# Performance work log

Hardware: AMD Instinct MI355X
Metric: run time of the kernel (lower is better)

Reference implementation:

```python
import jax, jax.numpy as jnp
import numpy as np
import math

B, T, V, A, D = 8, 128, 32000, 64, 256
NS, S, H = 16, 128, 4
HD = D // H
SCALE = math.sqrt(HD)


def _ln(x, g, b):
    m = x.mean(-1, keepdims=True)
    xc = x - m
    v = (xc * xc).mean(-1, keepdims=True)
    return xc * jax.lax.rsqrt(v + 1e-5) * g + b


def setup_inputs() -> dict:
    key = jax.random.key(0)
    ks = iter(jax.random.split(key, 64))
    def w(shape, s=0.02):
        return jax.random.normal(next(ks), shape, jnp.float32) * s
    return dict(
        idx=jax.random.randint(next(ks), (B, T), 0, V),
        emb=w((V, D)), pos=w((S, D)),
        Wsens=w((D, NS * D)), bsens=jnp.zeros((NS * D,), jnp.float32),
        Wfb=w((V, D)), bfb=jnp.zeros((D,), jnp.float32),
        Wfg=w((2 * D, D)), bfg=jnp.zeros((D,), jnp.float32),
        bind=w((NS, D)),
        anet=w((2, A, A)),
        Wg=w((2, 2 * D, D)), bg=jnp.zeros((2, D), jnp.float32),
        Wc=w((2, D, D)), bc=jnp.zeros((2, D), jnp.float32),
        lng=jnp.ones((2, D), jnp.float32), lnb=jnp.zeros((2, D), jnp.float32),
        cmix=jnp.ones((2,), jnp.float32) / 2, aimp=w((A,)),
        Wq=w((D, D)), bq=jnp.zeros((D,), jnp.float32),
        Wk=w((D, D)), bk=jnp.zeros((D,), jnp.float32),
        Wv=w((D, D)), bv=jnp.zeros((D,), jnp.float32),
        Wo=w((D, D)), bo=jnp.zeros((D,), jnp.float32),
        Wmg=w((2 * D, D)), bmg=jnp.zeros((D,), jnp.float32),
        mlng=jnp.ones((D,), jnp.float32), mlnb=jnp.zeros((D,), jnp.float32),
        Wa1=w((D, 2 * D)), ba1=jnp.zeros((2 * D,), jnp.float32),
        Wa2=w((2 * D, V)), ba2=jnp.zeros((V,), jnp.float32),
    )


def _forward(idx, emb, pos, Wsens, bsens, Wfb, bfb, Wfg, bfg, bind, anet,
             Wg, bg, Wc, bc, lng, lnb, cmix, aimp, Wq, bq, Wk, bk, Wv, bv,
             Wo, bo, Wmg, bmg, mlng, mlnb, Wa1, ba1, Wa2, ba2):
    percepts = emb[idx] + pos[:T][None]            # [B,T,D]
    iw = jax.nn.softmax(aimp)                      # [A]
    cw = jax.nn.softmax(cmix)                      # [2]
    sig_bind = jax.nn.sigmoid(bind)                # [NS,D]
    slot_ids = jnp.arange(S)

    def step(carry, pt):
        agents, prev_logits, mem, t = carry
        # feedback gating of percept
        fb = prev_logits @ Wfb + bfb
        fg = jax.nn.sigmoid(jnp.concatenate([fb, pt], -1) @ Wfg + bfg)
        mod = pt * (1 + fg)
        sens = (mod @ Wsens + bsens).reshape(B, NS, D) * sig_bind
        agents = agents.at[:, :NS].add(sens)
        # two swarm channels, mixed
        new = 0.
        for c in range(2):
            inter = jnp.einsum('ij,bjd->bid', anet[c], agents)
            cand = jax.nn.gelu(inter @ Wc[c] + bc[c], approximate=False)
            gate = jax.nn.sigmoid(jnp.concatenate([agents, inter], -1) @ Wg[c] + bg[c])
            new = new + cw[c] * _ln(gate * cand + (1 - gate) * agents, lng[c], lnb[c])
        agents = new
        cons = jnp.einsum('bad,a->bd', agents, iw)  # [B,D]
        # holographic memory attention over valid slots (< t)
        Q = (cons @ Wq + bq).reshape(B, 1, H, HD)
        K = (mem @ Wk + bk).reshape(B, S, H, HD)
        Vv = (mem @ Wv + bv).reshape(B, S, H, HD)
        scores = jnp.einsum('bqhd,bshd->bhqs', Q, K) / SCALE  # [B,H,1,S]
        valid = slot_ids < t
        scores = jnp.where(valid[None, None, None, :], scores, -1e9)
        attn = jax.nn.softmax(scores, -1)
        rec = jnp.einsum('bhqs,bshd->bqhd', attn, Vv).reshape(B, D)
        rec = rec @ Wo + bo
        mgate = jax.nn.sigmoid(jnp.concatenate([cons, rec], -1) @ Wmg + bmg)
        attended = _ln(cons + mgate * rec, mlng, mlnb)
        cons = jnp.where(t > 0, attended, cons)
        # write detached consensus to slot t (T == MEMORY_SLOTS)
        mem = jax.lax.dynamic_update_slice(
            mem, jax.lax.stop_gradient(cons)[:, None, :], (0, t, 0))
        h = jax.nn.gelu(cons @ Wa1 + ba1, approximate=False)
        logits = h @ Wa2 + ba2
        return (agents, jax.lax.stop_gradient(logits), mem, t + 1), logits

    carry0 = (jnp.zeros((B, A, D), jnp.float32),
              jnp.zeros((B, V), jnp.float32),
              jnp.zeros((B, S, D), jnp.float32),
              jnp.int32(0))
    _, logits = jax.lax.scan(step, carry0, percepts.transpose(1, 0, 2))
    return logits.transpose(1, 0, 2)  # [B,T,V]


def reference(idx, emb, pos, Wsens, bsens, Wfb, bfb, Wfg, bfg, bind, anet,
              Wg, bg, Wc, bc, lng, lnb, cmix, aimp, Wq, bq, Wk, bk, Wv, bv,
              Wo, bo, Wmg, bmg, mlng, mlnb, Wa1, ba1, Wa2, ba2):
    return _forward(idx, emb, pos, Wsens, bsens, Wfb, bfb, Wfg, bfg, bind,
                    anet, Wg, bg, Wc, bc, lng, lnb, cmix, aimp, Wq, bq, Wk,
                    bk, Wv, bv, Wo, bo, Wmg, bmg, mlng, mlnb, Wa1, ba1,
                    Wa2, ba2)
```

## Files before the change

kernel.cpp:

```cpp
#include <hip/hip_runtime.h>
#include <math.h>

#define DEV __device__ __forceinline__

constexpr int B = 8, T = 128, V = 32000, A = 64, D = 256, NS = 16, S = 128, H = 4, HD = 64;
constexpr int D2 = 2 * D;

DEV float sigm(float x) { return 1.0f / (1.0f + expf(-x)); }
DEV float geluf(float x) { return 0.5f * x * (1.0f + erff(x * 0.7071067811865476f)); }

DEV float blk_sum256(float v, float* red) {
  #pragma unroll
  for (int o = 32; o > 0; o >>= 1) v += __shfl_down(v, o, 64);
  int lane = threadIdx.x & 63, wid = threadIdx.x >> 6;
  __syncthreads();
  if (lane == 0) red[wid] = v;
  __syncthreads();
  return red[0] + red[1] + red[2] + red[3];
}


__global__ __launch_bounds__(256) void k_setup(const float* __restrict__ aimp,
                                               const float* __restrict__ cmix,
                                               const float* __restrict__ bind,
                                               float* __restrict__ iw, float* __restrict__ cwv,
                                               float* __restrict__ sigbind) {
  int tid = threadIdx.x;
  if (tid < 64) {
    float v = aimp[tid];
    float m = v;
    #pragma unroll
    for (int o = 32; o > 0; o >>= 1) m = fmaxf(m, __shfl_xor(m, o, 64));
    float e = expf(v - m);
    float s = e;
    #pragma unroll
    for (int o = 32; o > 0; o >>= 1) s += __shfl_xor(s, o, 64);
    iw[tid] = e / s;
  }
  if (tid == 0) {
    float a = cmix[0], b = cmix[1], m = fmaxf(a, b);
    float ea = expf(a - m), eb = expf(b - m);
    cwv[0] = ea / (ea + eb);
    cwv[1] = eb / (ea + eb);
  }
  for (int i = tid; i < NS * D; i += 256) sigbind[i] = sigm(bind[i]);
}

__global__ __launch_bounds__(256) void k_percepts(const int* __restrict__ idx,
                                                  const float* __restrict__ emb,
                                                  const float* __restrict__ pos,
                                                  float* __restrict__ P) {
  int i = blockIdx.x * 256 + threadIdx.x;
  if (i < B * T * D) {
    int d = i & (D - 1);
    int bt = i / D;
    int t = bt & (T - 1);
    P[i] = emb[(size_t)idx[bt] * D + d] + pos[t * D + d];
  }
}

__global__ __launch_bounds__(256) void k_cvec(const float* __restrict__ Wfb,
                                              const float* __restrict__ ba2,
                                              const float* __restrict__ bfb,
                                              float* __restrict__ cvec) {
  int j = blockIdx.x, tid = threadIdx.x;
  float s = 0.f;
  for (int v = tid; v < V; v += 256) s += ba2[v] * Wfb[(size_t)v * D + j];
  __shared__ float red[256];
  red[tid] = s;
  __syncthreads();
  for (int o = 128; o > 0; o >>= 1) {
    if (tid < o) red[tid] += red[tid + o];
    __syncthreads();
  }
  if (tid == 0) cvec[j] = red[0] + bfb[j];
}

__global__ __launch_bounds__(256) void k_mpart(const float* __restrict__ Wa2,
                                               const float* __restrict__ Wfb,
                                               float* __restrict__ part) {
  int it = blockIdx.y;
  int vc = blockIdx.x;
  int j = threadIdx.x;
  int i0 = it * 32, v0 = vc * 2000;
  __shared__ float a_l[32 * 125];
  float acc[32];
  #pragma unroll
  for (int r = 0; r < 32; r++) acc[r] = 0.f;
  for (int vb = 0; vb < 2000; vb += 125) {
    for (int l = threadIdx.x; l < 32 * 125; l += 256) {
      int r = l / 125, c = l - r * 125;
      a_l[l] = Wa2[(size_t)(i0 + r) * V + v0 + vb + c];
    }
    __syncthreads();
    for (int c = 0; c < 125; c++) {
      float w = Wfb[(size_t)(v0 + vb + c) * D + j];
      #pragma unroll
      for (int r = 0; r < 32; r++) acc[r] += a_l[r * 125 + c] * w;
    }
    __syncthreads();
  }
  for (int r = 0; r < 32; r++) part[((size_t)vc * D2 + i0 + r) * D + j] = acc[r];
}

__global__ __launch_bounds__(256) void k_mreduce(const float* __restrict__ part,
                                                 float* __restrict__ M) {
  int i = blockIdx.x, j = threadIdx.x;
  float s = 0.f;
  for (int vc = 0; vc < 16; vc++) s += part[((size_t)vc * D2 + i) * D + j];
  M[i * D + j] = s;
}

__global__ __launch_bounds__(256) void k_step0(const float* __restrict__ P,
                                               const float* __restrict__ bfb,
                                               const float* __restrict__ Wfg,
                                               const float* __restrict__ bfg,
                                               float* __restrict__ agents,
                                               float* __restrict__ mod) {
  int b = blockIdx.x, tid = threadIdx.x;
  for (int i = b * (A * D) + tid; i < (b + 1) * (A * D); i += 256) agents[i] = 0.f;
  __shared__ float cat[512];
  cat[tid] = bfb[tid];
  cat[256 + tid] = P[(b * T + 0) * D + tid];
  __syncthreads();
  float acc = bfg[tid];
  for (int k = 0; k < 512; k++) acc += cat[k] * Wfg[k * D + tid];
  float fg = sigm(acc);
  float pt = cat[256 + tid];
  mod[b * D + tid] = pt * (1.f + fg);
}


__global__ __launch_bounds__(256) void k_stepB(const float* __restrict__ Wsens,
                                               const float* __restrict__ bsens,
                                               const float* __restrict__ sigbind,
                                               const float* __restrict__ anet,
                                               const float* __restrict__ mod,
                                               float* __restrict__ agents,
                                               float* __restrict__ inter) {
  int b = blockIdx.y;
  int dc = blockIdx.x;
  int d0 = dc * 32;
  int tid = threadIdx.x;
  __shared__ float mod_l[256];
  __shared__ float ag_l[64][33];
  __shared__ float an_l[2 * 64 * 64];
  mod_l[tid] = mod[b * D + tid];
  for (int l = tid; l < 2 * 64 * 64; l += 256) an_l[l] = anet[l];
  for (int l = tid; l < 64 * 32; l += 256) {
    int j = l >> 5, dl = l & 31;
    ag_l[j][dl] = agents[(b * A + j) * D + d0 + dl];
  }
  __syncthreads();
  for (int l = tid; l < NS * 32; l += 256) {
    int j = l >> 5, dl = l & 31;
    int col = j * D + d0 + dl;
    float acc = bsens[col];
    for (int k = 0; k < D; k++) acc += mod_l[k] * Wsens[k * (NS * D) + col];
    float nv = ag_l[j][dl] + acc * sigbind[col];
    ag_l[j][dl] = nv;
    agents[(b * A + j) * D + d0 + dl] = nv;
  }
  __syncthreads();
  for (int l = tid; l < 2 * 64 * 32; l += 256) {
    int c = l >> 11;
    int rem = l & 2047;
    int i = rem >> 5, dl = rem & 31;
    const float* an = &an_l[(c * 64 + i) * 64];
    float acc = 0.f;
    #pragma unroll 8
    for (int j = 0; j < 64; j++) acc += an[j] * ag_l[j][dl];
    inter[(((c * B) + b) * A + i) * D + d0 + dl] = acc;
  }
}

__global__ __launch_bounds__(256) void k_stepC(const float* __restrict__ Wc,
                                               const float* __restrict__ bc,
                                               const float* __restrict__ Wg,
                                               const float* __restrict__ bg,
                                               const float* __restrict__ lng,
                                               const float* __restrict__ lnb,
                                               const float* __restrict__ cwv,
                                               const float* __restrict__ inter,
                                               float* __restrict__ agents) {
  int r0 = blockIdx.x * 4;
  int tid = threadIdx.x;
  __shared__ float ag_l[4][256];
  __shared__ float in_l[4][2][256];
  __shared__ float red[4];
  for (int rr = 0; rr < 4; rr++) {
    ag_l[rr][tid] = agents[(r0 + rr) * D + tid];
    in_l[rr][0][tid] = inter[(r0 + rr) * D + tid];
    in_l[rr][1][tid] = inter[B * A * D + (r0 + rr) * D + tid];
  }
  __syncthreads();
  float c0[4] = {0, 0, 0, 0}, c1[4] = {0, 0, 0, 0};
  float g0[4] = {0, 0, 0, 0}, g1[4] = {0, 0, 0, 0};
  for (int k = 0; k < 256; k++) {
    float wc0 = Wc[k * D + tid];
    float wc1 = Wc[D * D + k * D + tid];
    float wg0 = Wg[k * D + tid];
    float wg1 = Wg[D2 * D + k * D + tid];
    #pragma unroll
    for (int rr = 0; rr < 4; rr++) {
      c0[rr] += in_l[rr][0][k] * wc0;
      c1[rr] += in_l[rr][1][k] * wc1;
      g0[rr] += ag_l[rr][k] * wg0;
      g1[rr] += ag_l[rr][k] * wg1;
    }
  }
  for (int k = 0; k < 256; k++) {
    float wg0 = Wg[(256 + k) * D + tid];
    float wg1 = Wg[D2 * D + (256 + k) * D + tid];
    #pragma unroll
    for (int rr = 0; rr < 4; rr++) {
      g0[rr] += in_l[rr][0][k] * wg0;
      g1[rr] += in_l[rr][1][k] * wg1;
    }
  }
  float cw0 = cwv[0], cw1 = cwv[1];
  float bc0 = bc[tid], bc1 = bc[D + tid];
  float bg0 = bg[tid], bg1 = bg[D + tid];
  float lg0 = lng[tid], lg1 = lng[D + tid];
  float lb0 = lnb[tid], lb1 = lnb[D + tid];
  for (int rr = 0; rr < 4; rr++) {
    float cand0 = geluf(c0[rr] + bc0);
    float cand1 = geluf(c1[rr] + bc1);
    float gate0 = sigm(g0[rr] + bg0);
    float gate1 = sigm(g1[rr] + bg1);
    float a = ag_l[rr][tid];
    float v0 = gate0 * cand0 + (1.f - gate0) * a;
    float v1 = gate1 * cand1 + (1.f - gate1) * a;
    float s0 = blk_sum256(v0, red);
    float q0 = blk_sum256(v0 * v0, red);
    float s1 = blk_sum256(v1, red);
    float q1 = blk_sum256(v1 * v1, red);
    float m0 = s0 * (1.f / 256.f), var0 = q0 * (1.f / 256.f) - m0 * m0;
    float m1 = s1 * (1.f / 256.f), var1 = q1 * (1.f / 256.f) - m1 * m1;
    float ln0 = (v0 - m0) * rsqrtf(var0 + 1e-5f) * lg0 + lb0;
    float ln1 = (v1 - m1) * rsqrtf(var1 + 1e-5f) * lg1 + lb1;
    agents[(r0 + rr) * D + tid] = cw0 * ln0 + cw1 * ln1;
  }
}

__global__ __launch_bounds__(256) void k_stepD(
    int t, const float* __restrict__ P, const float* __restrict__ iw,
    const float* __restrict__ Wq, const float* __restrict__ bq,
    const float* __restrict__ Wk, const float* __restrict__ bk,
    const float* __restrict__ Wv, const float* __restrict__ bv,
    const float* __restrict__ Wo, const float* __restrict__ bo,
    const float* __restrict__ Wmg, const float* __restrict__ bmg,
    const float* __restrict__ mlng, const float* __restrict__ mlnb,
    const float* __restrict__ Wa1, const float* __restrict__ ba1,
    const float* __restrict__ M, const float* __restrict__ cvec,
    const float* __restrict__ Wfg, const float* __restrict__ bfg,
    const float* __restrict__ agents, float* __restrict__ Kc, float* __restrict__ Vc,
    float* __restrict__ Hall, float* __restrict__ mod) {
  int b = blockIdx.x, tid = threadIdx.x;
  __shared__ float cons_l[256], q_l[256], o_l[256], cf_l[256], h_l[512];
  __shared__ float sc_l[4][128];
  __shared__ float den_l[4];
  __shared__ float red[4];
  float acc = 0.f;
  for (int a = 0; a < A; a++) acc += iw[a] * agents[(b * A + a) * D + tid];
  cons_l[tid] = acc;
  __syncthreads();
  float consd = acc;
  float cfd;
  if (t > 0) {
    float q = bq[tid];
    for (int k = 0; k < 256; k++) q += cons_l[k] * Wq[k * D + tid];
    q_l[tid] = q;
    __syncthreads();
    for (int p = tid; p < 4 * 128; p += 256) {
      int h = p >> 7, s = p & 127;
      if (s < t) {
        const float* krow = &Kc[(b * S + s) * D + h * HD];
        const float* qh = &q_l[h * HD];
        float sc = 0.f;
        #pragma unroll 8
        for (int e = 0; e < HD; e++) sc += qh[e] * krow[e];
        sc_l[h][s] = sc * 0.125f;
      }
    }
    __syncthreads();
    int h = tid >> 6, lane = tid & 63;
    {
      float m = -1e30f;
      for (int s = lane; s < t; s += 64) m = fmaxf(m, sc_l[h][s]);
      #pragma unroll
      for (int o = 32; o > 0; o >>= 1) m = fmaxf(m, __shfl_xor(m, o, 64));
      float sum = 0.f;
      for (int s = lane; s < t; s += 64) {
        float e = expf(sc_l[h][s] - m);
        sc_l[h][s] = e;
        sum += e;
      }
      #pragma unroll
      for (int o = 32; o > 0; o >>= 1) sum += __shfl_xor(sum, o, 64);
      if (lane == 0) den_l[h] = sum;
    }
    __syncthreads();
    float r = 0.f;
    for (int s = 0; s < t; s++) r += sc_l[h][s] * Vc[(b * S + s) * D + tid];
    r /= den_l[h];
    __syncthreads();
    q_l[tid] = r;
    __syncthreads();
    float o = bo[tid];
    for (int k = 0; k < 256; k++) o += q_l[k] * Wo[k * D + tid];
    o_l[tid] = o;
    __syncthreads();
    float mg = bmg[tid];
    for (int k = 0; k < 256; k++) mg += cons_l[k] * Wmg[k * D + tid];
    for (int k = 0; k < 256; k++) mg += o_l[k] * Wmg[(256 + k) * D + tid];
    mg = sigm(mg);
    float val = consd + mg * o;
    float s1 = blk_sum256(val, red);
    float s2 = blk_sum256(val * val, red);
    float mean = s1 * (1.f / 256.f), var = s2 * (1.f / 256.f) - mean * mean;
    cfd = (val - mean) * rsqrtf(var + 1e-5f) * mlng[tid] + mlnb[tid];
  } else {
    cfd = consd;
  }
  __syncthreads();
  cf_l[tid] = cfd;
  __syncthreads();
  float kk = bk[tid], vv = bv[tid];
  for (int k = 0; k < 256; k++) {
    float c = cf_l[k];
    kk += c * Wk[k * D + tid];
    vv += c * Wv[k * D + tid];
  }
  Kc[(b * S + t) * D + tid] = kk;
  Vc[(b * S + t) * D + tid] = vv;
  for (int m = tid; m < 512; m += 256) {
    float hh = ba1[m];
    for (int k = 0; k < 256; k++) hh += cf_l[k] * Wa1[k * D2 + m];
    hh = geluf(hh);
    h_l[m] = hh;
    Hall[((size_t)b * T + t) * D2 + m] = hh;
  }
  __syncthreads();
  if (t < T - 1) {
    float fb = cvec[tid];
    for (int k = 0; k < 512; k++) fb += h_l[k] * M[k * D + tid];
    float ptn = P[(b * T + t + 1) * D + tid];
    q_l[tid] = fb;
    o_l[tid] = ptn;
    __syncthreads();
    float fg = bfg[tid];
    for (int k = 0; k < 256; k++) fg += q_l[k] * Wfg[k * D + tid];
    for (int k = 0; k < 256; k++) fg += o_l[k] * Wfg[(256 + k) * D + tid];
    fg = sigm(fg);
    mod[b * D + tid] = ptn * (1.f + fg);
  }
}

__global__ __launch_bounds__(256) void k_logits(const float* __restrict__ Hall,
                                                const float* __restrict__ Wa2,
                                                const float* __restrict__ ba2,
                                                float* __restrict__ out) {
  int rt = blockIdx.y;
  int v = blockIdx.x * 256 + threadIdx.x;
  const float* hrow = Hall + (size_t)rt * 32 * D2;
  float acc[32];
  float bb = ba2[v];
  #pragma unroll
  for (int r = 0; r < 32; r++) acc[r] = bb;
  for (int k = 0; k < D2; k++) {
    float w = Wa2[(size_t)k * V + v];
    #pragma unroll
    for (int r = 0; r < 32; r++) acc[r] += hrow[r * D2 + k] * w;
  }
  for (int r = 0; r < 32; r++) out[(size_t)(rt * 32 + r) * V + v] = acc[r];
}


extern "C" void kernel_launch(void* const* d_in, const int* in_sizes, int n_in,
                              void* d_out, int out_size, void* d_ws, size_t ws_size,
                              hipStream_t stream) {
  const int* idx = (const int*)d_in[0];
  const float* emb = (const float*)d_in[1];
  const float* pos = (const float*)d_in[2];
  const float* Wsens = (const float*)d_in[3];
  const float* bsens = (const float*)d_in[4];
  const float* Wfb = (const float*)d_in[5];
  const float* bfb = (const float*)d_in[6];
  const float* Wfg = (const float*)d_in[7];
  const float* bfg = (const float*)d_in[8];
  const float* bind = (const float*)d_in[9];
  const float* anet = (const float*)d_in[10];
  const float* Wg = (const float*)d_in[11];
  const float* bg = (const float*)d_in[12];
  const float* Wc = (const float*)d_in[13];
  const float* bc = (const float*)d_in[14];
  const float* lng = (const float*)d_in[15];
  const float* lnb = (const float*)d_in[16];
  const float* cmix = (const float*)d_in[17];
  const float* aimp = (const float*)d_in[18];
  const float* Wq = (const float*)d_in[19];
  const float* bq = (const float*)d_in[20];
  const float* Wk = (const float*)d_in[21];
  const float* bk = (const float*)d_in[22];
  const float* Wv = (const float*)d_in[23];
  const float* bv = (const float*)d_in[24];
  const float* Wo = (const float*)d_in[25];
  const float* bo = (const float*)d_in[26];
  const float* Wmg = (const float*)d_in[27];
  const float* bmg = (const float*)d_in[28];
  const float* mlng = (const float*)d_in[29];
  const float* mlnb = (const float*)d_in[30];
  const float* Wa1 = (const float*)d_in[31];
  const float* ba1 = (const float*)d_in[32];
  const float* Wa2 = (const float*)d_in[33];
  const float* ba2 = (const float*)d_in[34];

  float* ws = (float*)d_ws;
  float* M = ws;
  float* cvec = ws + 131072;
  float* iw = ws + 131328;
  float* cw = ws + 131392;
  float* sigbind = ws + 131456;
  float* P = ws + 135552;
  float* agents = ws + 397696;
  float* inter = ws + 528768;
  float* mod = ws + 790912;
  float* Kc = ws + 792960;
  float* Vc = ws + 1055104;
  float* Hall = ws + 1317248;
  float* Mpart = ws + 1841536;

  k_setup<<<1, 256, 0, stream>>>(aimp, cmix, bind, iw, cw, sigbind);
  k_percepts<<<dim3((B * T * D + 255) / 256), 256, 0, stream>>>(idx, emb, pos, P);
  k_cvec<<<256, 256, 0, stream>>>(Wfb, ba2, bfb, cvec);
  k_mpart<<<dim3(16, 16), 256, 0, stream>>>(Wa2, Wfb, Mpart);
  k_mreduce<<<512, 256, 0, stream>>>(Mpart, M);
  k_step0<<<B, 256, 0, stream>>>(P, bfb, Wfg, bfg, agents, mod);

  for (int t = 0; t < T; t++) {
    k_stepB<<<dim3(8, B), 256, 0, stream>>>(Wsens, bsens, sigbind, anet, mod, agents, inter);
    k_stepC<<<128, 256, 0, stream>>>(Wc, bc, Wg, bg, lng, lnb, cw, inter, agents);
    k_stepD<<<B, 256, 0, stream>>>(t, P, iw, Wq, bq, Wk, bk, Wv, bv, Wo, bo, Wmg, bmg,
                                   mlng, mlnb, Wa1, ba1, M, cvec, Wfg, bfg, agents, Kc, Vc,
                                   Hall, mod);
  }
  k_logits<<<dim3(125, 32), 256, 0, stream>>>(Hall, Wa2, ba2, (float*)d_out);
}
```

Before: 26.39 ms.

## Replace per-step kernel launches with a cooperative persistent kernel and prefolded weights

Swaps the 3×128 per-timestep kernel launches for a single cooperative persistent kernel of 256 blocks that uses grid.sync between phases. The work inside each step is spread over many more blocks. Weight products are folded ahead of time (M·Wfg, Wo·Wmg, P·Wfg, bias vectors) to shorten the serial chain, and K is stored transposed. The goal is to remove launch overhead and the poor parallelism of 8-block stages, at the cost of many grid-wide barriers per step and some reassociated floating-point arithmetic.

```diff
diff --git a/kernel.cpp b/kernel.cpp
--- a/kernel.cpp
+++ b/kernel.cpp
@@ -1,5 +1,8 @@
 #include <hip/hip_runtime.h>
+#include <hip/hip_cooperative_groups.h>
 #include <math.h>
+
+namespace cg = cooperative_groups;
 
 #define DEV __device__ __forceinline__
 
@@ -8,16 +11,6 @@
 
 DEV float sigm(float x) { return 1.0f / (1.0f + expf(-x)); }
 DEV float geluf(float x) { return 0.5f * x * (1.0f + erff(x * 0.7071067811865476f)); }
-
-DEV float blk_sum256(float v, float* red) {
-  #pragma unroll
-  for (int o = 32; o > 0; o >>= 1) v += __shfl_down(v, o, 64);
-  int lane = threadIdx.x & 63, wid = threadIdx.x >> 6;
-  __syncthreads();
-  if (lane == 0) red[wid] = v;
-  __syncthreads();
-  return red[0] + red[1] + red[2] + red[3];
-}
 
 
 __global__ __launch_bounds__(256) void k_setup(const float* __restrict__ aimp,
@@ -82,12 +75,12 @@
   int it = blockIdx.y;
   int vc = blockIdx.x;
   int j = threadIdx.x;
-  int i0 = it * 32, v0 = vc * 2000;
+  int i0 = it * 32, v0 = vc * 4000;
   __shared__ float a_l[32 * 125];
   float acc[32];
   #pragma unroll
   for (int r = 0; r < 32; r++) acc[r] = 0.f;
-  for (int vb = 0; vb < 2000; vb += 125) {
+  for (int vb = 0; vb < 4000; vb += 125) {
     for (int l = threadIdx.x; l < 32 * 125; l += 256) {
       int r = l / 125, c = l - r * 125;
       a_l[l] = Wa2[(size_t)(i0 + r) * V + v0 + vb + c];
@@ -107,253 +100,399 @@
                                                  float* __restrict__ M) {
   int i = blockIdx.x, j = threadIdx.x;
   float s = 0.f;
-  for (int vc = 0; vc < 16; vc++) s += part[((size_t)vc * D2 + i) * D + j];
+  for (int vc = 0; vc < 8; vc++) s += part[((size_t)vc * D2 + i) * D + j];
   M[i * D + j] = s;
 }
 
-__global__ __launch_bounds__(256) void k_step0(const float* __restrict__ P,
-                                               const float* __restrict__ bfb,
-                                               const float* __restrict__ Wfg,
-                                               const float* __restrict__ bfg,
-                                               float* __restrict__ agents,
-                                               float* __restrict__ mod) {
-  int b = blockIdx.x, tid = threadIdx.x;
-  for (int i = b * (A * D) + tid; i < (b + 1) * (A * D); i += 256) agents[i] = 0.f;
-  __shared__ float cat[512];
-  cat[tid] = bfb[tid];
-  cat[256 + tid] = P[(b * T + 0) * D + tid];
+__global__ __launch_bounds__(256) void k_gemmK256(const float* __restrict__ Am,
+                                                  const float* __restrict__ Bm,
+                                                  float* __restrict__ C, int I) {
+  int r0 = blockIdx.x * 8;
+  int tid = threadIdx.x;
+  __shared__ float a_l[8][256];
+  for (int i = tid; i < 8 * 256; i += 256) a_l[i >> 8][i & 255] = Am[(r0 + (i >> 8)) * 256 + (i & 255)];
   __syncthreads();
-  float acc = bfg[tid];
-  for (int k = 0; k < 512; k++) acc += cat[k] * Wfg[k * D + tid];
-  float fg = sigm(acc);
-  float pt = cat[256 + tid];
-  mod[b * D + tid] = pt * (1.f + fg);
-}
-
-
-__global__ __launch_bounds__(256) void k_stepB(const float* __restrict__ Wsens,
-                                               const float* __restrict__ bsens,
-                                               const float* __restrict__ sigbind,
-                                               const float* __restrict__ anet,
-                                               const float* __restrict__ mod,
-                                               float* __restrict__ agents,
-                                               float* __restrict__ inter) {
-  int b = blockIdx.y;
-  int dc = blockIdx.x;
-  int d0 = dc * 32;
+  float acc[8] = {0, 0, 0, 0, 0, 0, 0, 0};
+  for (int k = 0; k < 256; k++) {
+    float bv = Bm[k * 256 + tid];
+    #pragma unroll
+    for (int r = 0; r < 8; r++) acc[r] += a_l[r][k] * bv;
+  }
+  for (int r = 0; r < 8; r++) C[(r0 + r) * 256 + tid] = acc[r];
+}
+
+__global__ __launch_bounds__(256) void k_vecmat(const float* __restrict__ a,
+                                                const float* __restrict__ Bm,
+                                                const float* __restrict__ bias,
+                                                float* __restrict__ out) {
   int tid = threadIdx.x;
-  __shared__ float mod_l[256];
-  __shared__ float ag_l[64][33];
-  __shared__ float an_l[2 * 64 * 64];
-  mod_l[tid] = mod[b * D + tid];
-  for (int l = tid; l < 2 * 64 * 64; l += 256) an_l[l] = anet[l];
-  for (int l = tid; l < 64 * 32; l += 256) {
-    int j = l >> 5, dl = l & 31;
-    ag_l[j][dl] = agents[(b * A + j) * D + d0 + dl];
-  }
+  __shared__ float a_l[256];
+  a_l[tid] = a[tid];
   __syncthreads();
-  for (int l = tid; l < NS * 32; l += 256) {
-    int j = l >> 5, dl = l & 31;
-    int col = j * D + d0 + dl;
-    float acc = bsens[col];
-    for (int k = 0; k < D; k++) acc += mod_l[k] * Wsens[k * (NS * D) + col];
-    float nv = ag_l[j][dl] + acc * sigbind[col];
-    ag_l[j][dl] = nv;
-    agents[(b * A + j) * D + d0 + dl] = nv;
-  }
-  __syncthreads();
-  for (int l = tid; l < 2 * 64 * 32; l += 256) {
-    int c = l >> 11;
-    int rem = l & 2047;
-    int i = rem >> 5, dl = rem & 31;
-    const float* an = &an_l[(c * 64 + i) * 64];
-    float acc = 0.f;
-    #pragma unroll 8
-    for (int j = 0; j < 64; j++) acc += an[j] * ag_l[j][dl];
-    inter[(((c * B) + b) * A + i) * D + d0 + dl] = acc;
-  }
-}
-
-__global__ __launch_bounds__(256) void k_stepC(const float* __restrict__ Wc,
-                                               const float* __restrict__ bc,
-                                               const float* __restrict__ Wg,
-                                               const float* __restrict__ bg,
-                                               const float* __restrict__ lng,
-                                               const float* __restrict__ lnb,
-                                               const float* __restrict__ cwv,
-                                               const float* __restrict__ inter,
-                                               float* __restrict__ agents) {
-  int r0 = blockIdx.x * 4;
-  int tid = threadIdx.x;
-  __shared__ float ag_l[4][256];
-  __shared__ float in_l[4][2][256];
-  __shared__ float red[4];
-  for (int rr = 0; rr < 4; rr++) {
-    ag_l[rr][tid] = agents[(r0 + rr) * D + tid];
-    in_l[rr][0][tid] = inter[(r0 + rr) * D + tid];
-    in_l[rr][1][tid] = inter[B * A * D + (r0 + rr) * D + tid];
-  }
-  __syncthreads();
-  float c0[4] = {0, 0, 0, 0}, c1[4] = {0, 0, 0, 0};
-  float g0[4] = {0, 0, 0, 0}, g1[4] = {0, 0, 0, 0};
-  for (int k = 0; k < 256; k++) {
-    float wc0 = Wc[k * D + tid];
-    float wc1 = Wc[D * D + k * D + tid];
-    float wg0 = Wg[k * D + tid];
-    float wg1 = Wg[D2 * D + k * D + tid];
-    #pragma unroll
-    for (int rr = 0; rr < 4; rr++) {
-      c0[rr] += in_l[rr][0][k] * wc0;
-      c1[rr] += in_l[rr][1][k] * wc1;
-      g0[rr] += ag_l[rr][k] * wg0;
-      g1[rr] += ag_l[rr][k] * wg1;
-    }
-  }
-  for (int k = 0; k < 256; k++) {
-    float wg0 = Wg[(256 + k) * D + tid];
-    float wg1 = Wg[D2 * D + (256 + k) * D + tid];
-    #pragma unroll
-    for (int rr = 0; rr < 4; rr++) {
-      g0[rr] += in_l[rr][0][k] * wg0;
-      g1[rr] += in_l[rr][1][k] * wg1;
-    }
-  }
-  float cw0 = cwv[0], cw1 = cwv[1];
-  float bc0 = bc[tid], bc1 = bc[D + tid];
-  float bg0 = bg[tid], bg1 = bg[D + tid];
-  float lg0 = lng[tid], lg1 = lng[D + tid];
-  float lb0 = lnb[tid], lb1 = lnb[D + tid];
-  for (int rr = 0; rr < 4; rr++) {
-    float cand0 = geluf(c0[rr] + bc0);
-    float cand1 = geluf(c1[rr] + bc1);
-    float gate0 = sigm(g0[rr] + bg0);
-    float gate1 = sigm(g1[rr] + bg1);
-    float a = ag_l[rr][tid];
-    float v0 = gate0 * cand0 + (1.f - gate0) * a;
-    float v1 = gate1 * cand1 + (1.f - gate1) * a;
-    float s0 = blk_sum256(v0, red);
-    float q0 = blk_sum256(v0 * v0, red);
-    float s1 = blk_sum256(v1, red);
-    float q1 = blk_sum256(v1 * v1, red);
-    float m0 = s0 * (1.f / 256.f), var0 = q0 * (1.f / 256.f) - m0 * m0;
-    float m1 = s1 * (1.f / 256.f), var1 = q1 * (1.f / 256.f) - m1 * m1;
-    float ln0 = (v0 - m0) * rsqrtf(var0 + 1e-5f) * lg0 + lb0;
-    float ln1 = (v1 - m1) * rsqrtf(var1 + 1e-5f) * lg1 + lb1;
-    agents[(r0 + rr) * D + tid] = cw0 * ln0 + cw1 * ln1;
-  }
-}
-
-__global__ __launch_bounds__(256) void k_stepD(
-    int t, const float* __restrict__ P, const float* __restrict__ iw,
-    const float* __restrict__ Wq, const float* __restrict__ bq,
-    const float* __restrict__ Wk, const float* __restrict__ bk,
-    const float* __restrict__ Wv, const float* __restrict__ bv,
-    const float* __restrict__ Wo, const float* __restrict__ bo,
-    const float* __restrict__ Wmg, const float* __restrict__ bmg,
-    const float* __restrict__ mlng, const float* __restrict__ mlnb,
-    const float* __restrict__ Wa1, const float* __restrict__ ba1,
-    const float* __restrict__ M, const float* __restrict__ cvec,
-    const float* __restrict__ Wfg, const float* __restrict__ bfg,
-    const float* __restrict__ agents, float* __restrict__ Kc, float* __restrict__ Vc,
-    float* __restrict__ Hall, float* __restrict__ mod) {
-  int b = blockIdx.x, tid = threadIdx.x;
-  __shared__ float cons_l[256], q_l[256], o_l[256], cf_l[256], h_l[512];
-  __shared__ float sc_l[4][128];
-  __shared__ float den_l[4];
-  __shared__ float red[4];
   float acc = 0.f;
-  for (int a = 0; a < A; a++) acc += iw[a] * agents[(b * A + a) * D + tid];
-  cons_l[tid] = acc;
-  __syncthreads();
-  float consd = acc;
-  float cfd;
-  if (t > 0) {
-    float q = bq[tid];
-    for (int k = 0; k < 256; k++) q += cons_l[k] * Wq[k * D + tid];
-    q_l[tid] = q;
-    __syncthreads();
-    for (int p = tid; p < 4 * 128; p += 256) {
-      int h = p >> 7, s = p & 127;
-      if (s < t) {
-        const float* krow = &Kc[(b * S + s) * D + h * HD];
-        const float* qh = &q_l[h * HD];
-        float sc = 0.f;
+  for (int k = 0; k < 256; k++) acc += a_l[k] * Bm[k * 256 + tid];
+  out[tid] = acc + bias[tid];
+}
+
+
+struct PP {
+  const float *Wsens, *bsens, *sigbind, *anet, *Wc, *bc, *Wg, *bg, *lng, *lnb, *cw, *iw;
+  const float *Wq, *bq, *Wk, *bk, *Wv, *bv, *Wo, *bo, *Wmg, *WoMg, *cvec2, *mlng, *mlnb;
+  const float *Wa1, *ba1, *M2, *cvec3, *cvec4, *P, *pW;
+  float *agents, *u, *psum, *consbuf, *qbuf, *recraw, *val, *psumv, *hbuf, *mod, *KcT, *Vc, *Hall;
+};
+
+__global__ __launch_bounds__(512) void k_persist(PP p) {
+  cg::grid_group grid = cg::this_grid();
+  const int bid = blockIdx.x;
+  const int tid = threadIdx.x;
+  const int gsize = 256 * 512;
+  const int gid = bid * 512 + tid;
+
+  __shared__ float sm[10240];
+
+  for (int i = gid; i < B * A * D; i += gsize) p.agents[i] = 0.f;
+  for (int i = gid; i < B * D; i += gsize) {
+    int b = i >> 8, j = i & 255;
+    float fg = sigm(p.cvec4[j] + p.pW[(b * T + 0) * D + j]);
+    p.mod[i] = p.P[(b * T + 0) * D + j] * (1.f + fg);
+  }
+  grid.sync();
+
+  for (int t = 0; t < T; t++) {
+    {
+      int b = bid >> 5, g = bid & 31;
+      int c0 = g * 128;
+      float* mod_l = sm;
+      float* part = sm + 4096;
+      if (tid < 256) mod_l[tid] = p.mod[b * D + tid];
+      __syncthreads();
+      int kp = tid >> 7, cl = tid & 127;
+      int col = c0 + cl;
+      float acc = 0.f;
+      for (int kk = 0; kk < 64; kk++) {
+        int k = kp * 64 + kk;
+        acc += mod_l[k] * p.Wsens[k * (NS * D) + col];
+      }
+      part[kp * 128 + cl] = acc;
+      __syncthreads();
+      if (tid < 128) {
+        int c = c0 + tid;
+        float s = part[tid] + part[128 + tid] + part[256 + tid] + part[384 + tid];
+        float sens = (s + p.bsens[c]) * p.sigbind[c];
+        int j = c >> 8, d = c & 255;
+        p.agents[(b * A + j) * D + d] += sens;
+      }
+    }
+    grid.sync();
+
+    {
+      int rg = bid >> 3, cgp = bid & 7;
+      int b = rg >> 2, a0 = (rg & 3) * 16;
+      int ch = cgp >> 2, jc0 = (cgp & 3) * 64;
+      float* ag16 = sm;
+      float* inter_l = sm + 4096;
+      float* anet_l = sm + 8192;
+      float2* red2 = (float2*)(sm + 9216);
+      for (int i = tid; i < 4096; i += 512) ag16[i] = p.agents[(b * A + a0) * D + i];
+      for (int i = tid; i < 1024; i += 512) anet_l[i] = p.anet[ch * 4096 + a0 * 64 + i];
+      __syncthreads();
+      {
+        int d = tid & 255, rh = tid >> 8;
+        float acc[8];
+        #pragma unroll
+        for (int r = 0; r < 8; r++) acc[r] = 0.f;
+        for (int j = 0; j < 64; j++) {
+          float agv = p.agents[(b * A + j) * D + d];
+          #pragma unroll
+          for (int r = 0; r < 8; r++) acc[r] += anet_l[(rh * 8 + r) * 64 + j] * agv;
+        }
+        #pragma unroll
+        for (int r = 0; r < 8; r++) inter_l[(rh * 8 + r) * 256 + d] = acc[r];
+      }
+      __syncthreads();
+      {
+        int rr = tid >> 5, jp = tid & 31;
+        int j0 = jc0 + jp * 2;
+        const float2* Wc2 = (const float2*)(p.Wc + ch * 65536);
+        const float2* Wg2 = (const float2*)(p.Wg + ch * 131072);
+        float2 ca = {0.f, 0.f}, ga = {0.f, 0.f};
+        int jh = j0 >> 1;
+        for (int k = 0; k < 256; k++) {
+          float iv = inter_l[rr * 256 + k];
+          float av = ag16[rr * 256 + k];
+          float2 wc = Wc2[k * 128 + jh];
+          float2 wg = Wg2[k * 128 + jh];
+          ca.x += iv * wc.x; ca.y += iv * wc.y;
+          ga.x += av * wg.x; ga.y += av * wg.y;
+        }
+        for (int k = 0; k < 256; k++) {
+          float iv = inter_l[rr * 256 + k];
+          float2 wg = Wg2[(256 + k) * 128 + jh];
+          ga.x += iv * wg.x; ga.y += iv * wg.y;
+        }
+        int row = rg * 16 + rr;
+        float candx = geluf(ca.x + p.bc[ch * 256 + j0]);
+        float candy = geluf(ca.y + p.bc[ch * 256 + j0 + 1]);
+        float gatex = sigm(ga.x + p.bg[ch * 256 + j0]);
+        float gatey = sigm(ga.y + p.bg[ch * 256 + j0 + 1]);
+        float ax = ag16[rr * 256 + j0], ay = ag16[rr * 256 + j0 + 1];
+        float ux = gatex * candx + (1.f - gatex) * ax;
+        float uy = gatey * candy + (1.f - gatey) * ay;
+        ((float2*)p.u)[((ch * 512 + row) * 256 + j0) >> 1] = make_float2(ux, uy);
+        red2[tid] = make_float2(ux + uy, ux * ux + uy * uy);
+        __syncthreads();
+        if (jp == 0) {
+          float s = 0.f, q = 0.f;
+          #pragma unroll
+          for (int jj = 0; jj < 32; jj++) {
+            float2 v = red2[rr * 32 + jj];
+            s += v.x; q += v.y;
+          }
+          p.psum[((ch * 512 + row) * 4 + (cgp & 3)) * 2 + 0] = s;
+          p.psum[((ch * 512 + row) * 4 + (cgp & 3)) * 2 + 1] = q;
+        }
+      }
+    }
+    grid.sync();
+
+    {
+      int r = bid * 2 + (tid >> 8);
+      int j = tid & 255;
+      float s0 = 0.f, q0 = 0.f, s1 = 0.f, q1 = 0.f;
+      #pragma unroll
+      for (int cgi = 0; cgi < 4; cgi++) {
+        s0 += p.psum[((0 * 512 + r) * 4 + cgi) * 2 + 0];
+        q0 += p.psum[((0 * 512 + r) * 4 + cgi) * 2 + 1];
+        s1 += p.psum[((512 + r) * 4 + cgi) * 2 + 0];
+        q1 += p.psum[((512 + r) * 4 + cgi) * 2 + 1];
+      }
+      float u0 = p.u[(0 * 512 + r) * 256 + j];
+      float u1 = p.u[(512 + r) * 256 + j];
+      float m0 = s0 * (1.f / 256.f), v0 = q0 * (1.f / 256.f) - m0 * m0;
+      float m1 = s1 * (1.f / 256.f), v1 = q1 * (1.f / 256.f) - m1 * m1;
+      float ln0 = (u0 - m0) * rsqrtf(v0 + 1e-5f) * p.lng[j] + p.lnb[j];
+      float ln1 = (u1 - m1) * rsqrtf(v1 + 1e-5f) * p.lng[256 + j] + p.lnb[256 + j];
+      p.agents[r * 256 + j] = p.cw[0] * ln0 + p.cw[1] * ln1;
+    }
+    grid.sync();
+
+    if (bid < 32) {
+      int b = bid >> 2, cgp = bid & 3;
+      float* part = sm;
+      float* cons_l = sm + 1024;
+      {
+        int k = tid & 255, ap = tid >> 8;
+        float acc = 0.f;
+        for (int a = ap * 32; a < ap * 32 + 32; a++)
+          acc += p.iw[a] * p.agents[(b * A + a) * D + k];
+        part[ap * 256 + k] = acc;
+      }
+      __syncthreads();
+      if (tid < 256) {
+        cons_l[tid] = part[tid] + part[256 + tid];
+        if (cgp == 0) p.consbuf[b * 256 + tid] = cons_l[tid];
+      }
+      __syncthreads();
+      {
+        int cl = tid & 63, kp = tid >> 6;
+        int col = cgp * 64 + cl;
+        float acc = 0.f;
+        for (int k = kp * 32; k < kp * 32 + 32; k++) acc += cons_l[k] * p.Wq[k * 256 + col];
+        part[kp * 64 + cl] = acc;
+      }
+      __syncthreads();
+      if (tid < 64) {
+        int col = cgp * 64 + tid;
+        float s = 0.f;
+        #pragma unroll
+        for (int kp = 0; kp < 8; kp++) s += part[kp * 64 + tid];
+        p.qbuf[b * 256 + col] = s + p.bq[col];
+      }
+    }
+    grid.sync();
+
+    if (bid < 32 && t > 0) {
+      int b = bid >> 2, h = bid & 3;
+      float* q_l = sm;
+      float* sc_l = sm + 128;
+      float* den_l = sm + 512;
+      if (tid < 64) q_l[tid] = p.qbuf[b * 256 + h * 64 + tid];
+      __syncthreads();
+      if (tid < 128 && tid < t) {
+        int s = tid;
+        float acc = 0.f;
         #pragma unroll 8
-        for (int e = 0; e < HD; e++) sc += qh[e] * krow[e];
-        sc_l[h][s] = sc * 0.125f;
-      }
-    }
-    __syncthreads();
-    int h = tid >> 6, lane = tid & 63;
+        for (int e = 0; e < 64; e++) acc += q_l[e] * p.KcT[((b * 4 + h) * 64 + e) * 128 + s];
+        sc_l[s] = acc * 0.125f;
+      }
+      __syncthreads();
+      if (tid < 64) {
+        float m = -1e30f;
+        for (int s = tid; s < t; s += 64) m = fmaxf(m, sc_l[s]);
+        #pragma unroll
+        for (int o = 32; o > 0; o >>= 1) m = fmaxf(m, __shfl_xor(m, o, 64));
+        float den = 0.f;
+        for (int s = tid; s < t; s += 64) {
+          float e = expf(sc_l[s] - m);
+          sc_l[s] = e;
+          den += e;
+        }
+        #pragma unroll
+        for (int o = 32; o > 0; o >>= 1) den += __shfl_xor(den, o, 64);
+        if (tid == 0) den_l[0] = den;
+      }
+      __syncthreads();
+      if (tid < 64) {
+        int d = tid;
+        float acc = 0.f;
+        for (int s = 0; s < t; s++) acc += sc_l[s] * p.Vc[(b * S + s) * D + h * 64 + d];
+        p.recraw[b * 256 + h * 64 + d] = acc / den_l[0];
+      }
+    }
+    grid.sync();
+
+    if (bid < 64 && t > 0) {
+      int b = bid >> 3, cgp = bid & 7;
+      int j0 = cgp * 32;
+      float* rr_l = sm;
+      float* cons_l2 = sm + 256;
+      float* partO = sm + 1024;
+      float* partM = sm + 1536;
+      float* partW = sm + 2048;
+      float* vred = sm + 2560;
+      float* v2red = sm + 2600;
+      if (tid < 256) {
+        rr_l[tid] = p.recraw[b * 256 + tid];
+        cons_l2[tid] = p.consbuf[b * 256 + tid];
+      }
+      __syncthreads();
+      {
+        int cl = tid & 31, kp = tid >> 5;
+        int col = j0 + cl;
+        float aO = 0.f, aM = 0.f, aW = 0.f;
+        for (int k = kp * 16; k < kp * 16 + 16; k++) {
+          aO += rr_l[k] * p.Wo[k * 256 + col];
+          aM += cons_l2[k] * p.Wmg[k * 256 + col];
+          aW += rr_l[k] * p.WoMg[k * 256 + col];
+        }
+        partO[kp * 32 + cl] = aO;
+        partM[kp * 32 + cl] = aM;
+        partW[kp * 32 + cl] = aW;
+      }
+      __syncthreads();
+      if (tid < 32) {
+        int col = j0 + tid;
+        float o = p.bo[col], mgin = p.cvec2[col];
+        #pragma unroll
+        for (int kp = 0; kp < 16; kp++) {
+          o += partO[kp * 32 + tid];
+          mgin += partM[kp * 32 + tid] + partW[kp * 32 + tid];
+        }
+        float mg = sigm(mgin);
+        float vv = cons_l2[col] + mg * o;
+        p.val[b * 256 + col] = vv;
+        vred[tid] = vv;
+        v2red[tid] = vv * vv;
+      }
+      __syncthreads();
+      if (tid == 0) {
+        float s = 0.f, q = 0.f;
+        #pragma unroll
+        for (int i = 0; i < 32; i++) { s += vred[i]; q += v2red[i]; }
+        p.psumv[(b * 8 + cgp) * 2 + 0] = s;
+        p.psumv[(b * 8 + cgp) * 2 + 1] = q;
+      }
+    }
+    grid.sync();
+
     {
-      float m = -1e30f;
-      for (int s = lane; s < t; s += 64) m = fmaxf(m, sc_l[h][s]);
-      #pragma unroll
-      for (int o = 32; o > 0; o >>= 1) m = fmaxf(m, __shfl_xor(m, o, 64));
-      float sum = 0.f;
-      for (int s = lane; s < t; s += 64) {
-        float e = expf(sc_l[h][s] - m);
-        sc_l[h][s] = e;
-        sum += e;
-      }
-      #pragma unroll
-      for (int o = 32; o > 0; o >>= 1) sum += __shfl_xor(sum, o, 64);
-      if (lane == 0) den_l[h] = sum;
-    }
-    __syncthreads();
-    float r = 0.f;
-    for (int s = 0; s < t; s++) r += sc_l[h][s] * Vc[(b * S + s) * D + tid];
-    r /= den_l[h];
-    __syncthreads();
-    q_l[tid] = r;
-    __syncthreads();
-    float o = bo[tid];
-    for (int k = 0; k < 256; k++) o += q_l[k] * Wo[k * D + tid];
-    o_l[tid] = o;
-    __syncthreads();
-    float mg = bmg[tid];
-    for (int k = 0; k < 256; k++) mg += cons_l[k] * Wmg[k * D + tid];
-    for (int k = 0; k < 256; k++) mg += o_l[k] * Wmg[(256 + k) * D + tid];
-    mg = sigm(mg);
-    float val = consd + mg * o;
-    float s1 = blk_sum256(val, red);
-    float s2 = blk_sum256(val * val, red);
-    float mean = s1 * (1.f / 256.f), var = s2 * (1.f / 256.f) - mean * mean;
-    cfd = (val - mean) * rsqrtf(var + 1e-5f) * mlng[tid] + mlnb[tid];
-  } else {
-    cfd = consd;
-  }
-  __syncthreads();
-  cf_l[tid] = cfd;
-  __syncthreads();
-  float kk = bk[tid], vv = bv[tid];
-  for (int k = 0; k < 256; k++) {
-    float c = cf_l[k];
-    kk += c * Wk[k * D + tid];
-    vv += c * Wv[k * D + tid];
-  }
-  Kc[(b * S + t) * D + tid] = kk;
-  Vc[(b * S + t) * D + tid] = vv;
-  for (int m = tid; m < 512; m += 256) {
-    float hh = ba1[m];
-    for (int k = 0; k < 256; k++) hh += cf_l[k] * Wa1[k * D2 + m];
-    hh = geluf(hh);
-    h_l[m] = hh;
-    Hall[((size_t)b * T + t) * D2 + m] = hh;
-  }
-  __syncthreads();
-  if (t < T - 1) {
-    float fb = cvec[tid];
-    for (int k = 0; k < 512; k++) fb += h_l[k] * M[k * D + tid];
-    float ptn = P[(b * T + t + 1) * D + tid];
-    q_l[tid] = fb;
-    o_l[tid] = ptn;
-    __syncthreads();
-    float fg = bfg[tid];
-    for (int k = 0; k < 256; k++) fg += q_l[k] * Wfg[k * D + tid];
-    for (int k = 0; k < 256; k++) fg += o_l[k] * Wfg[(256 + k) * D + tid];
-    fg = sigm(fg);
-    mod[b * D + tid] = ptn * (1.f + fg);
+      int b = bid >> 5, cgp = bid & 31;
+      float* cf_l = sm;
+      float* part = sm + 1024;
+      if (tid < 256) {
+        float cfv;
+        if (t > 0) {
+          float vv = p.val[b * 256 + tid];
+          float s1 = 0.f, s2 = 0.f;
+          #pragma unroll
+          for (int g = 0; g < 8; g++) {
+            s1 += p.psumv[(b * 8 + g) * 2 + 0];
+            s2 += p.psumv[(b * 8 + g) * 2 + 1];
+          }
+          float m = s1 * (1.f / 256.f), var = s2 * (1.f / 256.f) - m * m;
+          cfv = (vv - m) * rsqrtf(var + 1e-5f) * p.mlng[tid] + p.mlnb[tid];
+        } else {
+          cfv = p.consbuf[b * 256 + tid];
+        }
+        cf_l[tid] = cfv;
+      }
+      __syncthreads();
+      {
+        int kp = tid >> 5, task = tid & 31;
+        float acc = 0.f;
+        if (task < 8) {
+          int col = cgp * 8 + task;
+          for (int k = kp * 16; k < kp * 16 + 16; k++) acc += cf_l[k] * p.Wk[k * 256 + col];
+        } else if (task < 16) {
+          int col = cgp * 8 + (task - 8);
+          for (int k = kp * 16; k < kp * 16 + 16; k++) acc += cf_l[k] * p.Wv[k * 256 + col];
+        } else {
+          int hc = cgp * 16 + (task - 16);
+          for (int k = kp * 16; k < kp * 16 + 16; k++) acc += cf_l[k] * p.Wa1[k * 512 + hc];
+        }
+        part[kp * 32 + task] = acc;
+      }
+      __syncthreads();
+      if (tid < 32) {
+        int task = tid;
+        float s = 0.f;
+        #pragma unroll
+        for (int kp = 0; kp < 16; kp++) s += part[kp * 32 + task];
+        if (task < 8) {
+          int col = cgp * 8 + task;
+          float kk = s + p.bk[col];
+          int h = col >> 6, e = col & 63;
+          p.KcT[((b * 4 + h) * 64 + e) * 128 + t] = kk;
+        } else if (task < 16) {
+          int col = cgp * 8 + (task - 8);
+          p.Vc[(b * S + t) * D + col] = s + p.bv[col];
+        } else {
+          int hc = cgp * 16 + (task - 16);
+          float hh = geluf(s + p.ba1[hc]);
+          p.hbuf[b * 512 + hc] = hh;
+          p.Hall[(size_t)(b * T + t) * D2 + hc] = hh;
+        }
+      }
+    }
+    grid.sync();
+
+    if (bid < 32 && t < T - 1) {
+      int b = bid >> 2, cgp = bid & 3;
+      float* h_l = sm;
+      float* part = sm + 1024;
+      h_l[tid] = p.hbuf[b * 512 + tid];
+      __syncthreads();
+      {
+        int cl = tid & 63, kp = tid >> 6;
+        int col = cgp * 64 + cl;
+        float acc = 0.f;
+        for (int k = kp * 64; k < kp * 64 + 64; k++) acc += h_l[k] * p.M2[k * 256 + col];
+        part[kp * 64 + cl] = acc;
+      }
+      __syncthreads();
+      if (tid < 64) {
+        int col = cgp * 64 + tid;
+        float s = 0.f;
+        #pragma unroll
+        for (int kp = 0; kp < 8; kp++) s += part[kp * 64 + tid];
+        s += p.cvec3[col] + p.pW[(b * T + t + 1) * D + col];
+        float fg = sigm(s);
+        float pt = p.P[(b * T + t + 1) * D + col];
+        p.mod[b * 256 + col] = pt * (1.f + fg);
+      }
+    }
+    grid.sync();
   }
 }
 
@@ -417,33 +556,58 @@
   const float* ba2 = (const float*)d_in[34];
 
   float* ws = (float*)d_ws;
-  float* M = ws;
-  float* cvec = ws + 131072;
-  float* iw = ws + 131328;
-  float* cw = ws + 131392;
-  float* sigbind = ws + 131456;
-  float* P = ws + 135552;
-  float* agents = ws + 397696;
-  float* inter = ws + 528768;
-  float* mod = ws + 790912;
-  float* Kc = ws + 792960;
-  float* Vc = ws + 1055104;
-  float* Hall = ws + 1317248;
-  float* Mpart = ws + 1841536;
-
-  k_setup<<<1, 256, 0, stream>>>(aimp, cmix, bind, iw, cw, sigbind);
+  float* M2 = ws;
+  float* WoMg = ws + 131072;
+  float* cvec = ws + 196608;
+  float* cvec2 = ws + 196864;
+  float* cvec3 = ws + 197120;
+  float* cvec4 = ws + 197376;
+  float* iw = ws + 197632;
+  float* cwb = ws + 197696;
+  float* sigbind = ws + 197760;
+  float* P = ws + 201856;
+  float* pW = ws + 464000;
+  float* agents = ws + 726144;
+  float* u = ws + 857216;
+  float* psum = ws + 1119360;
+  float* consbuf = ws + 1127552;
+  float* qbuf = ws + 1129600;
+  float* recraw = ws + 1131648;
+  float* val = ws + 1133696;
+  float* psumv = ws + 1135744;
+  float* hbuf = ws + 1135872;
+  float* mod = ws + 1139968;
+  float* KcT = ws + 1142016;
+  float* Vc = ws + 1404160;
+  float* Hall = ws + 1666304;
+  float* M = ws + 2190592;
+  float* Mpart = ws + 2321664;
+
+  k_setup<<<1, 256, 0, stream>>>(aimp, cmix, bind, iw, cwb, sigbind);
   k_percepts<<<dim3((B * T * D + 255) / 256), 256, 0, stream>>>(idx, emb, pos, P);
   k_cvec<<<256, 256, 0, stream>>>(Wfb, ba2, bfb, cvec);
-  k_mpart<<<dim3(16, 16), 256, 0, stream>>>(Wa2, Wfb, Mpart);
+  k_mpart<<<dim3(8, 16), 256, 0, stream>>>(Wa2, Wfb, Mpart);
   k_mreduce<<<512, 256, 0, stream>>>(Mpart, M);
-  k_step0<<<B, 256, 0, stream>>>(P, bfb, Wfg, bfg, agents, mod);
-
-  for (int t = 0; t < T; t++) {
-    k_stepB<<<dim3(8, B), 256, 0, stream>>>(Wsens, bsens, sigbind, anet, mod, agents, inter);
-    k_stepC<<<128, 256, 0, stream>>>(Wc, bc, Wg, bg, lng, lnb, cw, inter, agents);
-    k_stepD<<<B, 256, 0, stream>>>(t, P, iw, Wq, bq, Wk, bk, Wv, bv, Wo, bo, Wmg, bmg,
-                                   mlng, mlnb, Wa1, ba1, M, cvec, Wfg, bfg, agents, Kc, Vc,
-                                   Hall, mod);
-  }
+  k_gemmK256<<<64, 256, 0, stream>>>(M, Wfg, M2, 512);
+  k_gemmK256<<<32, 256, 0, stream>>>(Wo, Wmg + 65536, WoMg, 256);
+  k_gemmK256<<<128, 256, 0, stream>>>(P, Wfg + 65536, pW, 1024);
+  k_vecmat<<<1, 256, 0, stream>>>(bo, Wmg + 65536, bmg, cvec2);
+  k_vecmat<<<1, 256, 0, stream>>>(cvec, Wfg, bfg, cvec3);
+  k_vecmat<<<1, 256, 0, stream>>>(bfb, Wfg, bfg, cvec4);
+
+  PP prm;
+  prm.Wsens = Wsens; prm.bsens = bsens; prm.sigbind = sigbind; prm.anet = anet;
+  prm.Wc = Wc; prm.bc = bc; prm.Wg = Wg; prm.bg = bg; prm.lng = lng; prm.lnb = lnb;
+  prm.cw = cwb; prm.iw = iw; prm.Wq = Wq; prm.bq = bq; prm.Wk = Wk; prm.bk = bk;
+  prm.Wv = Wv; prm.bv = bv; prm.Wo = Wo; prm.bo = bo; prm.Wmg = Wmg; prm.WoMg = WoMg;
+  prm.cvec2 = cvec2; prm.mlng = mlng; prm.mlnb = mlnb; prm.Wa1 = Wa1; prm.ba1 = ba1;
+  prm.M2 = M2; prm.cvec3 = cvec3; prm.cvec4 = cvec4; prm.P = P; prm.pW = pW;
+  prm.agents = agents; prm.u = u; prm.psum = psum; prm.consbuf = consbuf;
+  prm.qbuf = qbuf; prm.recraw = recraw; prm.val = val; prm.psumv = psumv;
+  prm.hbuf = hbuf; prm.mod = mod; prm.KcT = KcT; prm.Vc = Vc; prm.Hall = Hall;
+
+  void* args[] = {&prm};
+  hipLaunchCooperativeKernel((void*)k_persist, dim3(256), dim3(512), args, 0, stream);
+
   k_logits<<<dim3(125, 32), 256, 0, stream>>>(Hall, Wa2, ba2, (float*)d_out);
 }
```

Measured after the change: 73.90 ms. 180% more time.
